# Kernel tuning notes

Measured on AMD Instinct MI355X. Metric: run time of the kernel, lower is better.

Reference implementation:

```python
import jax, jax.numpy as jnp
import numpy as np

SCALE = 1.0 / np.float32(64.0 ** 0.5)  # hardcoded in source, not sqrt(d)


def setup_inputs() -> dict:
    key = jax.random.key(0)
    k1, k2 = jax.random.split(key)
    B, S, D, O = 8, 2048, 768, 768
    x = jax.random.normal(k1, (B, S, D), dtype=jnp.float32)
    kernel = jax.random.normal(k2, (3, D, O), dtype=jnp.float32) * 0.02
    return {"x": x, "kernel": kernel}


def reference(x, kernel):
    # x: [B,S,D], kernel: [3,D,O]
    WQ = jnp.einsum('bsd,do->bso', x, kernel[0])
    WK = jnp.einsum('bsd,do->bso', x, kernel[1])
    WV = jnp.einsum('bsd,do->bso', x, kernel[2])
    QK = jnp.einsum('bqo,bko->bqk', WQ, WK) * SCALE  # [B,S,S]
    A = jax.nn.softmax(QK, axis=-1)
    return jnp.einsum('bqk,bko->bqo', A, WV)  # [B,S,O]
```

## Files before the change

### kernel.cpp

```cpp
#include <hip/hip_runtime.h>

typedef unsigned short u16;
typedef __attribute__((ext_vector_type(8))) short short8;
typedef __attribute__((ext_vector_type(4))) float f32x4;
typedef __attribute__((ext_vector_type(8))) unsigned short ushort8;
typedef __attribute__((ext_vector_type(4))) unsigned short ushort4v;

__device__ __forceinline__ u16 f2bf(float f) {
    unsigned int u = __float_as_uint(f);
    u += 0x7FFFu + ((u >> 16) & 1u);
    return (u16)(u >> 16);
}
__device__ __forceinline__ float bf2f(u16 h) {
    return __uint_as_float(((unsigned int)h) << 16);
}

template <int MODE>
__global__ __launch_bounds__(256, 3) void gemm_bt(
    const u16* __restrict__ A, const u16* __restrict__ B,
    void* __restrict__ O0, void* __restrict__ O1, void* __restrict__ O2,
    float alpha)
{
    constexpr int K   = (MODE == 2) ? 2048 : 768;
    constexpr int lda = (MODE == 2) ? 2048 : 768;
    constexpr int ldb = (MODE == 2) ? 2048 : 768;
    constexpr int ITERS = K / 32;

    __shared__ uint4 sA[2][512];
    __shared__ uint4 sB[2][512];

    const int f = blockIdx.x;
    const int xcd = f & 7;
    const int u = f >> 3;

    int tm, bn, cn, which = 0;
    long aoff = 0, boff = 0;
    if constexpr (MODE == 0) {
        const int c = u >> 4;
        const int rl = u & 15;
        tm = (xcd * 16 + rl) * 128;
        bn = c * 128;
        which = c / 6;
        cn = (c % 6) * 128;
    } else if constexpr (MODE == 1) {
        const int p = u >> 6, t = u & 63, c = t >> 2, rl = t & 3;
        tm = (p * 4 + rl) * 128;
        bn = cn = c * 128;
        aoff = (long)xcd * 2048 * 768;
        boff = aoff;
    } else {
        const int p = u / 12, t = u % 12, c = t >> 1, rl = t & 1;
        tm = (p * 2 + rl) * 128;
        bn = cn = c * 128;
        aoff = (long)xcd * 2048 * 2048;
        boff = (long)xcd * 768 * 2048;
    }

    const int tid  = threadIdx.x;
    const int lane = tid & 63;
    const int wave = tid >> 6;
    const int wr = wave >> 1;
    const int wc = wave & 1;

    f32x4 acc[4][4] = {};

    const int s0 = tid, s1 = tid + 256;
    const int r0 = s0 >> 2, kc0 = (s0 & 3) ^ ((r0 >> 1) & 3);
    const int r1 = s1 >> 2, kc1 = (s1 & 3) ^ ((r1 >> 1) & 3);
    const uint4* gA0 = (const uint4*)(A + aoff) + ((long)(tm + r0) * lda + kc0 * 8) / 8;
    const uint4* gA1 = (const uint4*)(A + aoff) + ((long)(tm + r1) * lda + kc1 * 8) / 8;
    const uint4* gB0 = (const uint4*)(B + boff) + ((long)(bn + r0) * ldb + kc0 * 8) / 8;
    const uint4* gB1 = (const uint4*)(B + boff) + ((long)(bn + r1) * ldb + kc1 * 8) / 8;

    const int swz = ((lane >> 4) ^ ((lane >> 1) & 3)) * 8;
    const int a_row = (wr * 64 + (lane & 15)) * 32;
    const int b_row = (wc * 64 + (lane & 15)) * 32;

    uint4 ra0 = gA0[0], ra1 = gA1[0], rb0 = gB0[0], rb1 = gB1[0];

#pragma unroll 2
    for (int it = 0; it < ITERS; ++it) {
        const int buf = it & 1;
        sA[buf][s0] = ra0;  sA[buf][s1] = ra1;
        sB[buf][s0] = rb0;  sB[buf][s1] = rb1;
        const int nk = (it + 1 < ITERS) ? (it + 1) * 4 : it * 4;
        ra0 = gA0[nk];  ra1 = gA1[nk];  rb0 = gB0[nk];  rb1 = gB1[nk];
        asm volatile("s_waitcnt lgkmcnt(0)\n\ts_barrier" ::: "memory");

        const u16* a_base = (const u16*)&sA[buf][0] + a_row + swz;
        const u16* b_base = (const u16*)&sB[buf][0] + b_row + swz;
        short8 a[4], b[4];
#pragma unroll
        for (int i = 0; i < 4; ++i) a[i] = *(const short8*)(a_base + i * 16 * 32);
#pragma unroll
        for (int j = 0; j < 4; ++j) b[j] = *(const short8*)(b_base + j * 16 * 32);
#pragma unroll
        for (int i = 0; i < 4; ++i)
#pragma unroll
            for (int j = 0; j < 4; ++j)
                acc[i][j] = __builtin_amdgcn_mfma_f32_16x16x32_bf16(
                    a[i], b[j], acc[i][j], 0, 0, 0);
    }

#pragma unroll
    for (int i = 0; i < 4; ++i) {
        const int row0 = tm + wr * 64 + i * 16 + ((lane >> 4) << 2);
#pragma unroll
        for (int j = 0; j < 4; ++j) {
            const int col = cn + wc * 64 + j * 16 + (lane & 15);
#pragma unroll
            for (int rr = 0; rr < 4; ++rr) {
                const int row = row0 + rr;
                const float val = acc[i][j][rr] * alpha;
                if constexpr (MODE == 0) {
                    if (which == 0)
                        ((u16*)O0)[(long)row * 768 + col] = f2bf(val);
                    else if (which == 1)
                        ((u16*)O1)[(long)row * 768 + col] = f2bf(val);
                    else
                        ((u16*)O2)[((long)(row >> 11) * 768 + col) * 2048 + (row & 2047)] = f2bf(val);
                } else if constexpr (MODE == 1) {
                    ((u16*)O0)[(long)xcd * 2048 * 2048 + (long)row * 2048 + col] = f2bf(val);
                } else {
                    ((float*)O0)[(long)xcd * 2048 * 768 + (long)row * 768 + col] = val;
                }
            }
        }
    }
}

__global__ __launch_bounds__(256) void cvt_x_kernel(
    const float4* __restrict__ x, ushort4v* __restrict__ out, int n4)
{
    int i = blockIdx.x * 256 + threadIdx.x;
    if (i < n4) {
        float4 f = x[i];
        ushort4v o;
        o.x = f2bf(f.x); o.y = f2bf(f.y); o.z = f2bf(f.z); o.w = f2bf(f.w);
        out[i] = o;
    }
}

__global__ __launch_bounds__(256) void cvt_w_kernel(
    const float* __restrict__ w, u16* __restrict__ wt)
{
    int i = blockIdx.x * 256 + threadIdx.x;
    int d = i % 768;
    int o = (i / 768) % 768;
    int m = i / (768 * 768);
    wt[i] = f2bf(w[((long)m * 768 + d) * 768 + o]);
}

__global__ __launch_bounds__(256) void softmax_kernel(u16* __restrict__ S)
{
    const long row = blockIdx.x;
    u16* p = S + row * 2048;
    const int t = threadIdx.x;
    const int lane = t & 63;
    const int wave = t >> 6;
    __shared__ float red[8];

    ushort8 raw = *(const ushort8*)(p + t * 8);
    float v[8];
    float m = -1e30f;
#pragma unroll
    for (int i = 0; i < 8; ++i) { v[i] = bf2f(raw[i]); m = fmaxf(m, v[i]); }
#pragma unroll
    for (int off = 1; off < 64; off <<= 1) m = fmaxf(m, __shfl_xor(m, off, 64));
    if (lane == 0) red[wave] = m;
    __syncthreads();
    m = fmaxf(fmaxf(red[0], red[1]), fmaxf(red[2], red[3]));

    float s = 0.f;
#pragma unroll
    for (int i = 0; i < 8; ++i) { v[i] = __expf(v[i] - m); s += v[i]; }
#pragma unroll
    for (int off = 1; off < 64; off <<= 1) s += __shfl_xor(s, off, 64);
    if (lane == 0) red[4 + wave] = s;
    __syncthreads();
    s = (red[4] + red[5]) + (red[6] + red[7]);

    const float inv = 1.0f / s;
    ushort8 out;
#pragma unroll
    for (int i = 0; i < 8; ++i) out[i] = f2bf(v[i] * inv);
    *(ushort8*)(p + t * 8) = out;
}

extern "C" void kernel_launch(void* const* d_in, const int* in_sizes, int n_in,
                              void* d_out, int out_size, void* d_ws, size_t ws_size,
                              hipStream_t stream)
{
    const float* x  = (const float*)d_in[0];
    const float* wk = (const float*)d_in[1];
    float* out = (float*)d_out;

    char* ws = (char*)d_ws;
    u16* xbf = (u16*)(ws);
    u16* wt  = (u16*)(ws + 25165824);
    u16* qbf = (u16*)(ws + 28704768);
    u16* kbf = (u16*)(ws + 53870592);
    u16* vt  = (u16*)(ws + 79036416);
    u16* S   = (u16*)(ws + 104202240);

    cvt_x_kernel<<<dim3(12288), dim3(256), 0, stream>>>(
        (const float4*)x, (ushort4v*)xbf, 3145728);
    cvt_w_kernel<<<dim3(6912), dim3(256), 0, stream>>>(wk, wt);

    gemm_bt<0><<<dim3(2304), dim3(256), 0, stream>>>(
        xbf, wt, qbf, kbf, vt, 1.0f);

    gemm_bt<1><<<dim3(2048), dim3(256), 0, stream>>>(
        qbf, kbf, S, nullptr, nullptr, 0.125f);

    softmax_kernel<<<dim3(16384), dim3(256), 0, stream>>>(S);

    gemm_bt<2><<<dim3(768), dim3(256), 0, stream>>>(
        S, vt, out, nullptr, nullptr, 1.0f);
}
```

Measured before the change: 375.2 us.

## Switch GEMM to 32x32x16 MFMA with padded LDS layout

Replaces the 16x16x32 bf16 MFMA tiling (4x4 accumulators per wave) with 32x32x16 MFMA (2x2 accumulators of 16 floats), splitting each 32-wide K slice into two 16-wide steps. The XOR-swizzled shared-memory layout is replaced by rows padded to 40 elements to avoid bank conflicts, and the epilogue is remapped to the 32x32 output layout. The occupancy hint is raised from 3 to 4 blocks. The goal is fewer LDS reads per MFMA and higher MFMA throughput, at the cost of more LDS per block and possible register pressure under the tighter launch bound.

```diff
diff --git a/kernel.cpp b/kernel.cpp
--- a/kernel.cpp
+++ b/kernel.cpp
@@ -2,7 +2,7 @@
 
 typedef unsigned short u16;
 typedef __attribute__((ext_vector_type(8))) short short8;
-typedef __attribute__((ext_vector_type(4))) float f32x4;
+typedef __attribute__((ext_vector_type(16))) float f32x16;
 typedef __attribute__((ext_vector_type(8))) unsigned short ushort8;
 typedef __attribute__((ext_vector_type(4))) unsigned short ushort4v;
 
@@ -16,7 +16,7 @@
 }
 
 template <int MODE>
-__global__ __launch_bounds__(256, 3) void gemm_bt(
+__global__ __launch_bounds__(256, 4) void gemm_bt(
     const u16* __restrict__ A, const u16* __restrict__ B,
     void* __restrict__ O0, void* __restrict__ O1, void* __restrict__ O2,
     float alpha)
@@ -25,9 +25,10 @@
     constexpr int lda = (MODE == 2) ? 2048 : 768;
     constexpr int ldb = (MODE == 2) ? 2048 : 768;
     constexpr int ITERS = K / 32;
-
-    __shared__ uint4 sA[2][512];
-    __shared__ uint4 sB[2][512];
+    constexpr int LDR = 40;
+
+    __shared__ u16 sA[2][128 * LDR];
+    __shared__ u16 sB[2][128 * LDR];
 
     const int f = blockIdx.x;
     const int xcd = f & 7;
@@ -62,56 +63,59 @@
     const int wr = wave >> 1;
     const int wc = wave & 1;
 
-    f32x4 acc[4][4] = {};
+    f32x16 acc[2][2] = {};
 
     const int s0 = tid, s1 = tid + 256;
-    const int r0 = s0 >> 2, kc0 = (s0 & 3) ^ ((r0 >> 1) & 3);
-    const int r1 = s1 >> 2, kc1 = (s1 & 3) ^ ((r1 >> 1) & 3);
+    const int r0 = s0 >> 2, kc0 = s0 & 3;
+    const int r1 = s1 >> 2, kc1 = s1 & 3;
     const uint4* gA0 = (const uint4*)(A + aoff) + ((long)(tm + r0) * lda + kc0 * 8) / 8;
     const uint4* gA1 = (const uint4*)(A + aoff) + ((long)(tm + r1) * lda + kc1 * 8) / 8;
     const uint4* gB0 = (const uint4*)(B + boff) + ((long)(bn + r0) * ldb + kc0 * 8) / 8;
     const uint4* gB1 = (const uint4*)(B + boff) + ((long)(bn + r1) * ldb + kc1 * 8) / 8;
-
-    const int swz = ((lane >> 4) ^ ((lane >> 1) & 3)) * 8;
-    const int a_row = (wr * 64 + (lane & 15)) * 32;
-    const int b_row = (wc * 64 + (lane & 15)) * 32;
+    const int wA0 = r0 * LDR + kc0 * 8, wA1 = r1 * LDR + kc1 * 8;
+
+    const int fr = (lane & 31) * LDR + (lane >> 5) * 8;
+    const int a_t0 = (wr * 64) * LDR + fr;
+    const int b_t0 = (wc * 64) * LDR + fr;
 
     uint4 ra0 = gA0[0], ra1 = gA1[0], rb0 = gB0[0], rb1 = gB1[0];
 
 #pragma unroll 2
     for (int it = 0; it < ITERS; ++it) {
         const int buf = it & 1;
-        sA[buf][s0] = ra0;  sA[buf][s1] = ra1;
-        sB[buf][s0] = rb0;  sB[buf][s1] = rb1;
+        *(uint4*)&sA[buf][wA0] = ra0;  *(uint4*)&sA[buf][wA1] = ra1;
+        *(uint4*)&sB[buf][wA0] = rb0;  *(uint4*)&sB[buf][wA1] = rb1;
         const int nk = (it + 1 < ITERS) ? (it + 1) * 4 : it * 4;
         ra0 = gA0[nk];  ra1 = gA1[nk];  rb0 = gB0[nk];  rb1 = gB1[nk];
         asm volatile("s_waitcnt lgkmcnt(0)\n\ts_barrier" ::: "memory");
 
-        const u16* a_base = (const u16*)&sA[buf][0] + a_row + swz;
-        const u16* b_base = (const u16*)&sB[buf][0] + b_row + swz;
-        short8 a[4], b[4];
-#pragma unroll
-        for (int i = 0; i < 4; ++i) a[i] = *(const short8*)(a_base + i * 16 * 32);
-#pragma unroll
-        for (int j = 0; j < 4; ++j) b[j] = *(const short8*)(b_base + j * 16 * 32);
-#pragma unroll
-        for (int i = 0; i < 4; ++i)
-#pragma unroll
-            for (int j = 0; j < 4; ++j)
-                acc[i][j] = __builtin_amdgcn_mfma_f32_16x16x32_bf16(
-                    a[i], b[j], acc[i][j], 0, 0, 0);
-    }
-
-#pragma unroll
-    for (int i = 0; i < 4; ++i) {
-        const int row0 = tm + wr * 64 + i * 16 + ((lane >> 4) << 2);
-#pragma unroll
-        for (int j = 0; j < 4; ++j) {
-            const int col = cn + wc * 64 + j * 16 + (lane & 15);
-#pragma unroll
-            for (int rr = 0; rr < 4; ++rr) {
-                const int row = row0 + rr;
-                const float val = acc[i][j][rr] * alpha;
+#pragma unroll
+        for (int s = 0; s < 2; ++s) {
+            short8 a[2], b[2];
+#pragma unroll
+            for (int t = 0; t < 2; ++t) {
+                a[t] = *(const short8*)&sA[buf][a_t0 + t * 32 * LDR + s * 16];
+                b[t] = *(const short8*)&sB[buf][b_t0 + t * 32 * LDR + s * 16];
+            }
+#pragma unroll
+            for (int t = 0; t < 2; ++t)
+#pragma unroll
+                for (int uu = 0; uu < 2; ++uu)
+                    acc[t][uu] = __builtin_amdgcn_mfma_f32_32x32x16_bf16(
+                        a[t], b[uu], acc[t][uu], 0, 0, 0);
+        }
+    }
+
+#pragma unroll
+    for (int t = 0; t < 2; ++t) {
+#pragma unroll
+        for (int uu = 0; uu < 2; ++uu) {
+            const int col = cn + wc * 64 + uu * 32 + (lane & 31);
+            const int rbase = tm + wr * 64 + t * 32 + ((lane >> 5) << 2);
+#pragma unroll
+            for (int reg = 0; reg < 16; ++reg) {
+                const int row = rbase + (reg & 3) + ((reg >> 2) << 3);
+                const float val = acc[t][uu][reg] * alpha;
                 if constexpr (MODE == 0) {
                     if (which == 0)
                         ((u16*)O0)[(long)row * 768 + col] = f2bf(val);
```

Result: no change. 374.9 us (-0.1%).
